# Optimization experiments

Measured on AMD Instinct MI355X. Metric: run time of the kernel, lower is better.

The kernel has to match this reference:

```python
import jax, jax.numpy as jnp
import numpy as np

B, H, W = 64, 250, 250
NUM_PROTOTYPES = 10
FC1_IN = 55815  # 15 * 61 * 61


def _conv(x, w, b, stride, pad):
    y = jax.lax.conv_general_dilated(
        x, w, (stride, stride), [(pad, pad), (pad, pad)],
        dimension_numbers=("NCHW", "OIHW", "NCHW"))
    return y + b[None, :, None, None]


def _maxpool2_s1(x):
    # MaxPool2d(kernel_size=2, stride=1), VALID
    return jax.lax.reduce_window(x, -jnp.inf, jax.lax.max,
                                 (1, 1, 2, 2), (1, 1, 1, 1), "VALID")


def setup_inputs() -> dict:
    key = jax.random.key(0)
    ks = jax.random.split(key, 16)
    f32 = jnp.float32
    def rn(k, shape, fan_in):
        return (jax.random.normal(k, shape, dtype=f32) / np.sqrt(fan_in)).astype(f32)
    return {
        "x": jax.random.normal(ks[0], (B, 3, H, W), dtype=f32),
        "conv1_w": rn(ks[1], (6, 3, 5, 5), 3 * 25),
        "conv1_b": jnp.zeros((6,), f32),
        "conv2_w": rn(ks[2], (15, 6, 3, 3), 6 * 9),
        "conv2_b": jnp.zeros((15,), f32),
        "fc1_w": rn(ks[3], (120, FC1_IN), FC1_IN),
        "fc1_b": jnp.zeros((120,), f32),
        "fc2_w": rn(ks[4], (84, 120), 120),
        "fc2_b": jnp.zeros((84,), f32),
        "fc3_w": rn(ks[5], (1, 84), 84),
        "fc3_b": jnp.zeros((1,), f32),
        "prototypes": jax.random.normal(ks[6], (NUM_PROTOTYPES, 1), dtype=f32),
        "kh_w": rn(ks[7], (1, NUM_PROTOTYPES), NUM_PROTOTYPES),
        "kh_b": jnp.zeros((1,), f32),
    }


def reference(x, conv1_w, conv1_b, conv2_w, conv2_b,
              fc1_w, fc1_b, fc2_w, fc2_b, fc3_w, fc3_b,
              prototypes, kh_w, kh_b):
    # Dropout layers are identity at inference.
    h = jax.nn.relu(_conv(x, conv1_w, conv1_b, stride=2, pad=1))  # [B,6,124,124]
    h = _maxpool2_s1(h)                                           # [B,6,123,123]
    h = jax.nn.relu(_conv(h, conv2_w, conv2_b, stride=2, pad=1))  # [B,15,62,62]
    h = _maxpool2_s1(h)                                           # [B,15,61,61]
    h = h.reshape(h.shape[0], -1)                                 # [B,55815]
    h = jax.nn.relu(h @ fc1_w.T + fc1_b)
    h = jax.nn.relu(h @ fc2_w.T + fc2_b)
    z = h @ fc3_w.T + fc3_b                                       # [B,1]
    # Quantum kernel closed form: 4 wires each apply RY(z) then RY(-p);
    # |<0000|psi>| = prod_i cos((z - p)/2) = cos((z - p)/2)^4.
    kernel_sim = jnp.cos((z - prototypes[:, 0][None, :]) * 0.5) ** 4  # [B,P]
    logits = kernel_sim @ kh_w.T + kh_b                           # [B,1]
    probs = jax.nn.sigmoid(logits)
    return jnp.concatenate([probs, 1.0 - probs], axis=-1)         # [B,2]
```

## Files before the change

kernel.cpp:

```cpp
#include <hip/hip_runtime.h>
#include <hip/hip_bf16.h>
#include <math.h>


#define KTOT 55815
#define KTOT_PAD 55872
#define P1H 123
#define P2H 61
#define KC 64
#define KSPAN 128
#define NCHUNK 437

__global__ __launch_bounds__(256) void conv1_pool(
    const float* __restrict__ x, const float* __restrict__ w,
    const float* __restrict__ bias, float* __restrict__ out) {
  __shared__ float smem[6 * 16 * 65];
  const int b = blockIdx.y;
  const int ytile = blockIdx.x >> 1, xtile = blockIdx.x & 1;
  const int cy_base = 15 * ytile;
  const int cx_base = xtile ? 62 : 0;
  const int tid = threadIdx.x;
  const int ry = tid >> 4;
  const int st = tid & 15;
  const int gy0 = 2 * cy_base - 1;
  const int s0 = 2 * cx_base - 4;
  const float* xb = x + b * 187500;

  float acc[6][4];
#pragma unroll
  for (int oc = 0; oc < 6; ++oc) {
    const float bv = bias[oc];
#pragma unroll
    for (int p = 0; p < 4; ++p) acc[oc][p] = bv;
  }

  float4 rr[5];
  {
    const float* xc = xb;
#pragma unroll
    for (int s = 0; s < 5; ++s) {
      const int idx = tid + 256 * s;
      float4 v = {0.f, 0.f, 0.f, 0.f};
      if (idx < 35 * 34) {
        const int row = idx / 34, j = idx - row * 34;
        const int gy = gy0 + row, gx = s0 + 4 * j;
        if (gy >= 0 && gy < 250) {
          const float* rp = xc + gy * 250;
          if (gx >= 0 && gx + 3 < 250) {
            v = *reinterpret_cast<const float4*>(rp + gx);
          } else if (gx + 3 >= 0 && gx < 250) {
            v.x = (gx + 0 >= 0 && gx + 0 < 250) ? rp[gx + 0] : 0.f;
            v.y = (gx + 1 >= 0 && gx + 1 < 250) ? rp[gx + 1] : 0.f;
            v.z = (gx + 2 >= 0 && gx + 2 < 250) ? rp[gx + 2] : 0.f;
            v.w = (gx + 3 >= 0 && gx + 3 < 250) ? rp[gx + 3] : 0.f;
          }
        }
      }
      rr[s] = v;
    }
  }

  for (int ic = 0; ic < 3; ++ic) {
    __syncthreads();
#pragma unroll
    for (int s = 0; s < 5; ++s) {
      const int idx = tid + 256 * s;
      if (idx < 35 * 34) {
        const int row = idx / 34, j = idx - row * 34;
        const int gj = j ^ ((j >> 3) & 1);
        *reinterpret_cast<float4*>(&smem[row * 136 + 4 * gj]) = rr[s];
      }
    }
    __syncthreads();
    if (ic < 2) {
      const float* xc = xb + (ic + 1) * 62500;
#pragma unroll
      for (int s = 0; s < 5; ++s) {
        const int idx = tid + 256 * s;
        float4 v = {0.f, 0.f, 0.f, 0.f};
        if (idx < 35 * 34) {
          const int row = idx / 34, j = idx - row * 34;
          const int gy = gy0 + row, gx = s0 + 4 * j;
          if (gy >= 0 && gy < 250) {
            const float* rp = xc + gy * 250;
            if (gx >= 0 && gx + 3 < 250) {
              v = *reinterpret_cast<const float4*>(rp + gx);
            } else if (gx + 3 >= 0 && gx < 250) {
              v.x = (gx + 0 >= 0 && gx + 0 < 250) ? rp[gx + 0] : 0.f;
              v.y = (gx + 1 >= 0 && gx + 1 < 250) ? rp[gx + 1] : 0.f;
              v.z = (gx + 2 >= 0 && gx + 2 < 250) ? rp[gx + 2] : 0.f;
              v.w = (gx + 3 >= 0 && gx + 3 < 250) ? rp[gx + 3] : 0.f;
            }
          }
        }
        rr[s] = v;
      }
    }
#pragma unroll
    for (int ky = 0; ky < 5; ++ky) {
      const int row = 2 * ry + ky;
      float r16[16];
#pragma unroll
      for (int q = 0; q < 4; ++q) {
        const int c = 2 * st + q;
        const int gc = c ^ ((c >> 3) & 1);
        const float4 v =
            *reinterpret_cast<const float4*>(&smem[row * 136 + 4 * gc]);
        r16[4 * q + 0] = v.x; r16[4 * q + 1] = v.y;
        r16[4 * q + 2] = v.z; r16[4 * q + 3] = v.w;
      }
#pragma unroll
      for (int oc = 0; oc < 6; ++oc)
#pragma unroll
        for (int kx = 0; kx < 5; ++kx) {
          const float wv = w[oc * 75 + ic * 25 + ky * 5 + kx];
#pragma unroll
          for (int p = 0; p < 4; ++p)
            acc[oc][p] = fmaf(r16[2 * p + 3 + kx], wv, acc[oc][p]);
        }
    }
  }

  __syncthreads();
#pragma unroll
  for (int oc = 0; oc < 6; ++oc)
#pragma unroll
    for (int p = 0; p < 4; ++p)
      smem[(oc * 16 + ry) * 65 + 4 * st + p] = fmaxf(acc[oc][p], 0.f);
  __syncthreads();

  for (int idx = tid; idx < 15 * 63; idx += 256) {
    const int pyl = idx / 63, pxl = idx % 63;
    const int py = cy_base + pyl;
    const int px = cx_base + pxl;
    if (py > 122) continue;
    if (xtile == 1 && (pxl == 0 || px > 122)) continue;
    float* ob = out + ((size_t)(b * P1H + py) * P1H + px) * 6;
    float v[6];
#pragma unroll
    for (int oc = 0; oc < 6; ++oc) {
      const float* c0 = &smem[(oc * 16 + pyl) * 65];
      const float* c1 = &smem[(oc * 16 + pyl + 1) * 65];
      v[oc] = fmaxf(fmaxf(c0[pxl], c0[pxl + 1]), fmaxf(c1[pxl], c1[pxl + 1]));
    }
    float2 o0 = {v[0], v[1]}, o1 = {v[2], v[3]}, o2 = {v[4], v[5]};
    *reinterpret_cast<float2*>(ob + 0) = o0;
    *reinterpret_cast<float2*>(ob + 2) = o1;
    *reinterpret_cast<float2*>(ob + 4) = o2;
  }
}

__global__ __launch_bounds__(256, 2) void conv2_pool(
    const float* __restrict__ in, const float* __restrict__ w,
    const float* __restrict__ bias, float* __restrict__ A) {
  __shared__ float cs[15][16][16];
  const int b = blockIdx.y;
  const int ty = blockIdx.x / 5, tx = blockIdx.x % 5;
  const int py0 = ty * 15, px0 = tx * 15;
  const int tid = threadIdx.x;
  const int cyl = tid >> 4, cxl = tid & 15;
  const int cy = py0 + cyl, cx = px0 + cxl;
  const float* ib = in + (size_t)b * (P1H * P1H * 6);
  const bool cv = (cy < 62) && (cx < 62);
  const int iy0 = 2 * cy - 1, ix0 = 2 * cx - 1;

  float rin[54];
#pragma unroll
  for (int ky = 0; ky < 3; ++ky) {
    const int iy = iy0 + ky;
#pragma unroll
    for (int kx = 0; kx < 3; ++kx) {
      const int ix = ix0 + kx;
      const int e = (ky * 3 + kx) * 6;
      const bool ok = cv && (iy >= 0) && (iy < P1H) && (ix >= 0) && (ix < P1H);
      if (ok) {
        const float* p = ib + ((size_t)iy * P1H + ix) * 6;
        const float2 v0 = *reinterpret_cast<const float2*>(p + 0);
        const float2 v1 = *reinterpret_cast<const float2*>(p + 2);
        const float2 v2 = *reinterpret_cast<const float2*>(p + 4);
        rin[e + 0] = v0.x; rin[e + 1] = v0.y; rin[e + 2] = v1.x;
        rin[e + 3] = v1.y; rin[e + 4] = v2.x; rin[e + 5] = v2.y;
      } else {
        rin[e + 0] = 0.f; rin[e + 1] = 0.f; rin[e + 2] = 0.f;
        rin[e + 3] = 0.f; rin[e + 4] = 0.f; rin[e + 5] = 0.f;
      }
    }
  }
#pragma unroll
  for (int oc = 0; oc < 15; ++oc) {
    float a = bias[oc];
#pragma unroll
    for (int ic = 0; ic < 6; ++ic)
#pragma unroll
      for (int ky = 0; ky < 3; ++ky)
#pragma unroll
        for (int kx = 0; kx < 3; ++kx)
          a = fmaf(rin[(ky * 3 + kx) * 6 + ic],
                   w[oc * 54 + ic * 9 + ky * 3 + kx], a);
    cs[oc][cyl][cxl] = fmaxf(a, 0.f);
  }
  __syncthreads();
  if (tid < 225) {
    const int pyl = tid / 15, pxl = tid % 15;
    const int py = py0 + pyl, px = px0 + pxl;
    if (py < P2H && px < P2H) {
      float* ob = A + (size_t)b * KTOT_PAD;
#pragma unroll
      for (int oc = 0; oc < 15; ++oc) {
        const float v = fmaxf(fmaxf(cs[oc][pyl][pxl], cs[oc][pyl][pxl + 1]),
                              fmaxf(cs[oc][pyl + 1][pxl], cs[oc][pyl + 1][pxl + 1]));
        ob[oc * (P2H * P2H) + py * P2H + px] = v;
      }
    }
  }
}

__global__ __launch_bounds__(256) void fc1_partial(
    const float* __restrict__ A, const float* __restrict__ W,
    float* __restrict__ part) {
  __shared__ float As[64 * KC];
  __shared__ float Ws[120 * KC];
  const int tid = threadIdx.x;
  const int chunk = blockIdx.x;
  const int lane = tid & 63;
  const int wave = __builtin_amdgcn_readfirstlane(tid >> 6);
  const int mg = lane >> 3, ng = lane & 7;
  const int n0 = wave * 32;

  float acc[8][4];
#pragma unroll
  for (int r = 0; r < 8; ++r)
#pragma unroll
    for (int s = 0; s < 4; ++s) acc[r][s] = 0.0f;

  for (int half = 0; half < 2; ++half) {
    const int k0 = chunk * KSPAN + half * KC;
    const bool full = (k0 + KC <= KTOT);
    __syncthreads();

    for (int idx = tid; idx < 64 * 16; idx += 256) {
      const int m = idx >> 4, j = idx & 15;
      const int kg = k0 + 4 * j;
      float4 v;
      if (full || kg + 3 < KTOT) {
        v = *reinterpret_cast<const float4*>(A + (size_t)m * KTOT_PAD + kg);
      } else {
        v.x = (kg + 0 < KTOT) ? A[(size_t)m * KTOT_PAD + kg + 0] : 0.f;
        v.y = (kg + 1 < KTOT) ? A[(size_t)m * KTOT_PAD + kg + 1] : 0.f;
        v.z = (kg + 2 < KTOT) ? A[(size_t)m * KTOT_PAD + kg + 2] : 0.f;
        v.w = (kg + 3 < KTOT) ? A[(size_t)m * KTOT_PAD + kg + 3] : 0.f;
      }
      const int slot = (j & 8) | ((j & 7) ^ ((m >> 3) & 7));
      *reinterpret_cast<float4*>(&As[m * KC + 4 * slot]) = v;
    }
    if (full) {
      for (int idx = tid; idx < 120 * KC; idx += 256) {
        const int n = idx >> 6, k = idx & 63;
        const int j = k >> 2, q = k & 3;
        const int slot = (j & 8) | ((j & 7) ^ ((n >> 2) & 7));
        Ws[n * KC + 4 * slot + q] = W[(size_t)n * KTOT + k0 + k];
      }
    } else {
      for (int idx = tid; idx < 120 * KC; idx += 256) {
        const int n = idx >> 6, k = idx & 63;
        const int j = k >> 2, q = k & 3;
        const int slot = (j & 8) | ((j & 7) ^ ((n >> 2) & 7));
        const int kg = k0 + k;
        Ws[n * KC + 4 * slot + q] = (kg < KTOT) ? W[(size_t)n * KTOT + kg] : 0.f;
      }
    }
    __syncthreads();

    const float* Abase = As + mg * 8 * KC;
    const float* Wbase = Ws + (n0 + ng * 4) * KC;
#pragma unroll
    for (int k4 = 0; k4 < KC / 4; ++k4) {
      const int sA = 4 * ((k4 & 8) | ((k4 & 7) ^ mg));
      const int sW = 4 * ((k4 & 8) | ((k4 & 7) ^ ng));
      float4 a[8], wv[4];
#pragma unroll
      for (int r = 0; r < 8; ++r)
        a[r] = *reinterpret_cast<const float4*>(Abase + r * KC + sA);
#pragma unroll
      for (int s = 0; s < 4; ++s)
        wv[s] = *reinterpret_cast<const float4*>(Wbase + s * KC + sW);
#pragma unroll
      for (int r = 0; r < 8; ++r)
#pragma unroll
        for (int s = 0; s < 4; ++s) {
          float t = acc[r][s];
          t = fmaf(a[r].x, wv[s].x, t);
          t = fmaf(a[r].y, wv[s].y, t);
          t = fmaf(a[r].z, wv[s].z, t);
          t = fmaf(a[r].w, wv[s].w, t);
          acc[r][s] = t;
        }
    }
  }

  if (n0 + 4 * ng <= 116) {
    float* pb = part + (size_t)chunk * 7680 + n0 + 4 * ng;
#pragma unroll
    for (int r = 0; r < 8; ++r) {
      const float4 v = {acc[r][0], acc[r][1], acc[r][2], acc[r][3]};
      *reinterpret_cast<float4*>(pb + (mg * 8 + r) * 120) = v;
    }
  }
}

__global__ __launch_bounds__(256) void fc1_reduce(
    const float* __restrict__ part, const float* __restrict__ bias,
    float* __restrict__ h1) {
  __shared__ float red[8][32];
  const int tid = threadIdx.x;
  const int q = tid >> 5, l = tid & 31;
  const int t = blockIdx.x * 32 + l;
  float s = 0.0f;
  for (int c = q; c < NCHUNK; c += 8) s += part[(size_t)c * 7680 + t];
  red[q][l] = s;
  __syncthreads();
  if (q == 0) {
    float v = red[0][l] + red[1][l] + red[2][l] + red[3][l] +
              red[4][l] + red[5][l] + red[6][l] + red[7][l] + bias[t % 120];
    h1[t] = fmaxf(v, 0.0f);
  }
}

__global__ __launch_bounds__(256) void fc2_kernel(
    const float* __restrict__ h1, const float* __restrict__ W,
    const float* __restrict__ bias, float* __restrict__ h2) {
  __shared__ float hs[64][121];
  const int tid = threadIdx.x;
  for (int i = tid; i < 7680; i += 256) hs[i / 120][i % 120] = h1[i];
  __syncthreads();
  const int m = tid & 63;
  const int j = blockIdx.x * 4 + __builtin_amdgcn_readfirstlane(tid >> 6);
  const float* wj = W + j * 120;
  float a = bias[j];
  for (int k = 0; k < 120; ++k) a = fmaf(hs[m][k], wj[k], a);
  h2[m * 84 + j] = fmaxf(a, 0.0f);
}

__global__ void final_kernel(
    const float* __restrict__ h2, const float* __restrict__ w3,
    const float* __restrict__ b3, const float* __restrict__ proto,
    const float* __restrict__ khw, const float* __restrict__ khb,
    float* __restrict__ out) {
  const int m = threadIdx.x;
  const float* h = h2 + m * 84;
  float z = b3[0];
  for (int k = 0; k < 84; ++k) z = fmaf(h[k], w3[k], z);
  float logit = khb[0];
#pragma unroll
  for (int p = 0; p < 10; ++p) {
    const float c = cosf((z - proto[p]) * 0.5f);
    const float c2 = c * c;
    logit = fmaf(c2 * c2, khw[p], logit);
  }
  const float pr = 1.0f / (1.0f + expf(-logit));
  out[m * 2 + 0] = pr;
  out[m * 2 + 1] = 1.0f - pr;
}

extern "C" void kernel_launch(void* const* d_in, const int* in_sizes, int n_in,
                              void* d_out, int out_size, void* d_ws, size_t ws_size,
                              hipStream_t stream) {
  const float* x    = (const float*)d_in[0];
  const float* w1   = (const float*)d_in[1];
  const float* b1   = (const float*)d_in[2];
  const float* w2   = (const float*)d_in[3];
  const float* b2   = (const float*)d_in[4];
  const float* fw1  = (const float*)d_in[5];
  const float* fb1  = (const float*)d_in[6];
  const float* fw2  = (const float*)d_in[7];
  const float* fb2  = (const float*)d_in[8];
  const float* fw3  = (const float*)d_in[9];
  const float* fb3  = (const float*)d_in[10];
  const float* prot = (const float*)d_in[11];
  const float* khw  = (const float*)d_in[12];
  const float* khb  = (const float*)d_in[13];
  float* out = (float*)d_out;

  float* ws = (float*)d_ws;
  float* pool1 = ws;
  float* part  = ws;
  float* A     = ws + 5809536;
  float* h1    = A + 3575808;
  float* h2    = h1 + 7680;

  conv1_pool <<<dim3(18, 64), 256, 0, stream>>>(x, w1, b1, pool1);
  conv2_pool <<<dim3(25, 64), 256, 0, stream>>>(pool1, w2, b2, A);
  fc1_partial<<<dim3(NCHUNK), 256, 0, stream>>>(A, fw1, part);
  fc1_reduce <<<dim3(240), 256, 0, stream>>>(part, fb1, h1);
  fc2_kernel <<<dim3(21), 256, 0, stream>>>(h1, fw2, fb2, h2);
  final_kernel<<<dim3(1), 64, 0, stream>>>(h2, fw3, fb3, prot, khw, khb, out);
}
```

Measured before the change: 112.3 us.

## Compute two conv1 output rows per thread to reuse shared-memory input rows

```diff
diff --git a/kernel.cpp b/kernel.cpp
--- a/kernel.cpp
+++ b/kernel.cpp
@@ -14,34 +14,36 @@
 __global__ __launch_bounds__(256) void conv1_pool(
     const float* __restrict__ x, const float* __restrict__ w,
     const float* __restrict__ bias, float* __restrict__ out) {
-  __shared__ float smem[6 * 16 * 65];
+  __shared__ float smem[6 * 32 * 65];
   const int b = blockIdx.y;
   const int ytile = blockIdx.x >> 1, xtile = blockIdx.x & 1;
-  const int cy_base = 15 * ytile;
+  const int cy_base = 31 * ytile;
   const int cx_base = xtile ? 62 : 0;
   const int tid = threadIdx.x;
-  const int ry = tid >> 4;
+  const int q = tid >> 4;
   const int st = tid & 15;
   const int gy0 = 2 * cy_base - 1;
   const int s0 = 2 * cx_base - 4;
   const float* xb = x + b * 187500;
-
-  float acc[6][4];
+  const int cyA = cy_base + 2 * q;
+  const bool vA = (cyA < 124), vB = (cyA + 1 < 124);
+
+  float accA[6][4], accB[6][4];
 #pragma unroll
   for (int oc = 0; oc < 6; ++oc) {
     const float bv = bias[oc];
 #pragma unroll
-    for (int p = 0; p < 4; ++p) acc[oc][p] = bv;
-  }
-
-  float4 rr[5];
+    for (int p = 0; p < 4; ++p) { accA[oc][p] = bv; accB[oc][p] = bv; }
+  }
+
+  float4 rr[9];
   {
     const float* xc = xb;
 #pragma unroll
-    for (int s = 0; s < 5; ++s) {
+    for (int s = 0; s < 9; ++s) {
       const int idx = tid + 256 * s;
       float4 v = {0.f, 0.f, 0.f, 0.f};
-      if (idx < 35 * 34) {
+      if (idx < 67 * 34) {
         const int row = idx / 34, j = idx - row * 34;
         const int gy = gy0 + row, gx = s0 + 4 * j;
         if (gy >= 0 && gy < 250) {
@@ -63,9 +65,9 @@
   for (int ic = 0; ic < 3; ++ic) {
     __syncthreads();
 #pragma unroll
-    for (int s = 0; s < 5; ++s) {
+    for (int s = 0; s < 9; ++s) {
       const int idx = tid + 256 * s;
-      if (idx < 35 * 34) {
+      if (idx < 67 * 34) {
         const int row = idx / 34, j = idx - row * 34;
         const int gj = j ^ ((j >> 3) & 1);
         *reinterpret_cast<float4*>(&smem[row * 136 + 4 * gj]) = rr[s];
@@ -75,10 +77,10 @@
     if (ic < 2) {
       const float* xc = xb + (ic + 1) * 62500;
 #pragma unroll
-      for (int s = 0; s < 5; ++s) {
+      for (int s = 0; s < 9; ++s) {
         const int idx = tid + 256 * s;
         float4 v = {0.f, 0.f, 0.f, 0.f};
-        if (idx < 35 * 34) {
+        if (idx < 67 * 34) {
           const int row = idx / 34, j = idx - row * 34;
           const int gy = gy0 + row, gx = s0 + 4 * j;
           if (gy >= 0 && gy < 250) {
@@ -97,27 +99,44 @@
       }
     }
 #pragma unroll
-    for (int ky = 0; ky < 5; ++ky) {
-      const int row = 2 * ry + ky;
+    for (int ii = 0; ii < 7; ++ii) {
+      const int row = 4 * q + ii;
       float r16[16];
 #pragma unroll
-      for (int q = 0; q < 4; ++q) {
-        const int c = 2 * st + q;
+      for (int qq = 0; qq < 4; ++qq) {
+        const int c = 2 * st + qq;
         const int gc = c ^ ((c >> 3) & 1);
         const float4 v =
             *reinterpret_cast<const float4*>(&smem[row * 136 + 4 * gc]);
-        r16[4 * q + 0] = v.x; r16[4 * q + 1] = v.y;
-        r16[4 * q + 2] = v.z; r16[4 * q + 3] = v.w;
-      }
-#pragma unroll
-      for (int oc = 0; oc < 6; ++oc)
-#pragma unroll
-        for (int kx = 0; kx < 5; ++kx) {
-          const float wv = w[oc * 75 + ic * 25 + ky * 5 + kx];
-#pragma unroll
-          for (int p = 0; p < 4; ++p)
-            acc[oc][p] = fmaf(r16[2 * p + 3 + kx], wv, acc[oc][p]);
+        r16[4 * qq + 0] = v.x; r16[4 * qq + 1] = v.y;
+        r16[4 * qq + 2] = v.z; r16[4 * qq + 3] = v.w;
+      }
+      if (ii <= 4) {
+#pragma unroll
+        for (int oc = 0; oc < 6; ++oc) {
+          const float* wp = w + oc * 75 + ic * 25 + ii * 5;
+#pragma unroll
+          for (int kx = 0; kx < 5; ++kx) {
+            const float wv = wp[kx];
+#pragma unroll
+            for (int p = 0; p < 4; ++p)
+              accA[oc][p] = fmaf(r16[2 * p + 3 + kx], wv, accA[oc][p]);
+          }
         }
+      }
+      if (ii >= 2) {
+#pragma unroll
+        for (int oc = 0; oc < 6; ++oc) {
+          const float* wp = w + oc * 75 + ic * 25 + (ii - 2) * 5;
+#pragma unroll
+          for (int kx = 0; kx < 5; ++kx) {
+            const float wv = wp[kx];
+#pragma unroll
+            for (int p = 0; p < 4; ++p)
+              accB[oc][p] = fmaf(r16[2 * p + 3 + kx], wv, accB[oc][p]);
+          }
+        }
+      }
     }
   }
 
@@ -125,11 +144,15 @@
 #pragma unroll
   for (int oc = 0; oc < 6; ++oc)
 #pragma unroll
-    for (int p = 0; p < 4; ++p)
-      smem[(oc * 16 + ry) * 65 + 4 * st + p] = fmaxf(acc[oc][p], 0.f);
+    for (int p = 0; p < 4; ++p) {
+      smem[(oc * 32 + 2 * q + 0) * 65 + 4 * st + p] =
+          vA ? fmaxf(accA[oc][p], 0.f) : 0.f;
+      smem[(oc * 32 + 2 * q + 1) * 65 + 4 * st + p] =
+          vB ? fmaxf(accB[oc][p], 0.f) : 0.f;
+    }
   __syncthreads();
 
-  for (int idx = tid; idx < 15 * 63; idx += 256) {
+  for (int idx = tid; idx < 31 * 63; idx += 256) {
     const int pyl = idx / 63, pxl = idx % 63;
     const int py = cy_base + pyl;
     const int px = cx_base + pxl;
@@ -139,8 +162,8 @@
     float v[6];
 #pragma unroll
     for (int oc = 0; oc < 6; ++oc) {
-      const float* c0 = &smem[(oc * 16 + pyl) * 65];
-      const float* c1 = &smem[(oc * 16 + pyl + 1) * 65];
+      const float* c0 = &smem[(oc * 32 + pyl) * 65];
+      const float* c1 = &smem[(oc * 32 + pyl + 1) * 65];
       v[oc] = fmaxf(fmaxf(c0[pxl], c0[pxl + 1]), fmaxf(c1[pxl], c1[pxl + 1]));
     }
     float2 o0 = {v[0], v[1]}, o1 = {v[2], v[3]}, o2 = {v[4], v[5]};
@@ -388,7 +411,7 @@
   float* h1    = A + 3575808;
   float* h2    = h1 + 7680;
 
-  conv1_pool <<<dim3(18, 64), 256, 0, stream>>>(x, w1, b1, pool1);
+  conv1_pool <<<dim3(8, 64), 256, 0, stream>>>(x, w1, b1, pool1);
   conv2_pool <<<dim3(25, 64), 256, 0, stream>>>(pool1, w2, b2, A);
   fc1_partial<<<dim3(NCHUNK), 256, 0, stream>>>(A, fw1, part);
   fc1_reduce <<<dim3(240), 256, 0, stream>>>(part, fb1, h1);
```

Measured after the change: 110.0 us, median of 2. 1.02x faster.
